# Kernel tuning notes

Measured on AMD Instinct MI355X. Metric: run time of the kernel, lower is better.

## Reference

```python
import jax, jax.numpy as jnp
import numpy as np

D_MODEL = 1024
NUM_HEADS = 16
D_K = D_MODEL // NUM_HEADS


def setup_inputs() -> dict:
    key = jax.random.key(0)
    ks = jax.random.split(key, 9)
    s = 1.0 / np.sqrt(D_MODEL)
    x = jax.random.normal(ks[0], (2, 2048, D_MODEL), dtype=jnp.float32)
    Wq = jax.random.uniform(ks[1], (D_MODEL, D_MODEL), jnp.float32, -s, s)
    bq = jax.random.uniform(ks[2], (D_MODEL,), jnp.float32, -s, s)
    Wk = jax.random.uniform(ks[3], (D_MODEL, D_MODEL), jnp.float32, -s, s)
    bk = jax.random.uniform(ks[4], (D_MODEL,), jnp.float32, -s, s)
    Wv = jax.random.uniform(ks[5], (D_MODEL, D_MODEL), jnp.float32, -s, s)
    bv = jax.random.uniform(ks[6], (D_MODEL,), jnp.float32, -s, s)
    Wo = jax.random.uniform(ks[7], (D_MODEL, D_MODEL), jnp.float32, -s, s)
    bo = jax.random.uniform(ks[8], (D_MODEL,), jnp.float32, -s, s)
    return {"x": x, "Wq": Wq, "bq": bq, "Wk": Wk, "bk": bk,
            "Wv": Wv, "bv": bv, "Wo": Wo, "bo": bo}


def reference(x, Wq, bq, Wk, bk, Wv, bv, Wo, bo):
    B, S, _ = x.shape
    # torch Linear: y = x @ W.T + b
    def proj(W, b):
        h = x @ W.T + b                       # [B,S,D]
        return h.reshape(B, S, NUM_HEADS, D_K).transpose(0, 2, 1, 3)  # [B,H,S,Dk]
    Q = proj(Wq, bq)
    K = proj(Wk, bk)
    V = proj(Wv, bv)
    scale = 1.0 / np.sqrt(D_K)
    scores = jnp.einsum('bhqd,bhkd->bhqk', Q, K) * scale   # [B,H,S,S]
    causal = jnp.triu(jnp.ones((S, S), dtype=bool), k=1)   # True above diag
    scores = jnp.where(causal, -jnp.inf, scores)
    probs = jax.nn.softmax(scores, axis=-1)
    out = jnp.einsum('bhqk,bhkd->bhqd', probs, V)          # [B,H,S,Dk]
    out = out.transpose(0, 2, 1, 3).reshape(B, S, NUM_HEADS * D_K)
    return out @ Wo.T + bo
```

## Files before the change

kernel.cpp:

```cpp
#include <hip/hip_runtime.h>

typedef unsigned short u16;
typedef __attribute__((ext_vector_type(8))) short short8;
typedef __attribute__((ext_vector_type(4))) float floatx4;

__device__ __forceinline__ u16 f2bf(float x){
  union { float f; unsigned u; } v; v.f = x;
  unsigned r = v.u + 0x7fffu + ((v.u >> 16) & 1u);
  return (u16)(r >> 16);
}

__device__ __forceinline__ unsigned cvt_pk_bf16(float lo, float hi){
  unsigned r;
  asm("v_cvt_pk_bf16_f32 %0, %1, %2" : "=v"(r) : "v"(lo), "v"(hi));
  return r;
}

__device__ __forceinline__ float exp2_raw(float x){
  float r;
  asm("v_exp_f32 %0, %1" : "=v"(r) : "v"(x));
  return r;
}

__device__ __forceinline__ void gld16(const u16* g, u16* l){
  __builtin_amdgcn_global_load_lds(
      (const __attribute__((address_space(1))) void*)g,
      (__attribute__((address_space(3))) void*)l, 16, 0, 0);
}

#define WAIT_BAR_V4() asm volatile("s_waitcnt vmcnt(4) lgkmcnt(0)\ns_barrier" ::: "memory")
#define WAIT_BAR_V3() asm volatile("s_waitcnt vmcnt(3) lgkmcnt(0)\ns_barrier" ::: "memory")
#define WAIT_BAR_V0() asm volatile("s_waitcnt vmcnt(0) lgkmcnt(0)\ns_barrier" ::: "memory")

__global__ void k_cvt_all(const float* __restrict__ x,
                          const float* __restrict__ wq, const float* __restrict__ wk,
                          const float* __restrict__ wv, const float* __restrict__ wo,
                          u16* __restrict__ xb, u16* __restrict__ wqb, u16* __restrict__ wkb,
                          u16* __restrict__ wvb, u16* __restrict__ wob){
  const int i = blockIdx.x * 256 + threadIdx.x;
  const float* s; u16* d; int off;
  if (i < 1048576) { s = x; d = xb; off = i; }
  else {
    const int j = i - 1048576;
    const int wsel = j >> 18;
    off = j & 262143;
    s = (wsel==0) ? wq : (wsel==1) ? wk : (wsel==2) ? wv : wo;
    d = (wsel==0) ? wqb : (wsel==1) ? wkb : (wsel==2) ? wvb : wob;
  }
  const float4 f = ((const float4*)s)[off];
  unsigned lo = (unsigned)f2bf(f.x) | ((unsigned)f2bf(f.y) << 16);
  unsigned hi = (unsigned)f2bf(f.z) | ((unsigned)f2bf(f.w) << 16);
  ((uint2*)d)[off] = make_uint2(lo, hi);
}

__global__ __launch_bounds__(256) void k_gemm_qkv(
    const u16* __restrict__ A,
    const u16* __restrict__ Wq, const u16* __restrict__ Wk, const u16* __restrict__ Wv,
    const float* __restrict__ bq, const float* __restrict__ bk, const float* __restrict__ bv,
    u16* __restrict__ Qo, u16* __restrict__ Ko, u16* __restrict__ Vo)
{
  const int bid = (int)blockIdx.x;
  const int xcd = bid & 7;
  const int i5  = bid >> 3;
  const int xb_ = ((xcd >> 2) << 2) + (i5 & 3);
  const int rest = i5 >> 2;
  const int yb_ = ((xcd & 3) << 3) + (rest & 7);
  const int mode = rest >> 3;

  const u16* W      = (mode==1) ? Wk : (mode==2) ? Wv : Wq;
  const float* bias = (mode==1) ? bk : (mode==2) ? bv : bq;

  __shared__ u16 lA[3][4096];
  __shared__ u16 lB[3][4096];

  const int tid  = threadIdx.x;
  const int row0 = yb_ * 128;
  const int col0 = xb_ * 128;

  const int srow = tid >> 2;
  const int sgp  = tid & 3;
  const int sgl  = sgp ^ ((srow >> 1) & 3);
  const u16* ga0 = A + (row0 + srow)      * 1024 + sgl * 8;
  const u16* ga1 = A + (row0 + srow + 64) * 1024 + sgl * 8;
  const u16* gb0 = W + (col0 + srow)      * 1024 + sgl * 8;
  const u16* gb1 = W + (col0 + srow + 64) * 1024 + sgl * 8;

  const int l  = tid & 63, w = tid >> 6;
  const int wr = w >> 1,  wc = w & 1;
  const int lr = l & 15,  grp = l >> 4;
  const int sw = (lr >> 1) & 3;
  int aoff[4], boff[4];
#pragma unroll
  for (int m = 0; m < 4; ++m) aoff[m] = (wr*64 + m*16 + lr)*32 + ((grp ^ sw) * 8);
#pragma unroll
  for (int n = 0; n < 4; ++n) boff[n] = (wc*64 + n*16 + lr)*32 + ((grp ^ sw) * 8);

  floatx4 acc[4][4];
#pragma unroll
  for (int m = 0; m < 4; ++m)
#pragma unroll
    for (int n = 0; n < 4; ++n) acc[m][n] = (floatx4){0.f, 0.f, 0.f, 0.f};

#define STAGE(buf, kt_) do { \
    const int k0_ = (kt_) * 32; \
    gld16(ga0 + k0_, &lA[(buf)][tid*8]); \
    gld16(ga1 + k0_, &lA[(buf)][2048 + tid*8]); \
    gld16(gb0 + k0_, &lB[(buf)][tid*8]); \
    gld16(gb1 + k0_, &lB[(buf)][2048 + tid*8]); \
  } while (0)

  STAGE(0, 0);
  STAGE(1, 1);
  asm volatile("s_waitcnt vmcnt(4)\ns_barrier" ::: "memory");

  for (int kt0 = 0; kt0 < 32; kt0 += 3) {
#pragma unroll
    for (int i = 0; i < 3; ++i) {
      const int kt = kt0 + i;
      if (kt >= 32) break;
      const bool st2 = (kt + 2 < 32);
      if (st2) STAGE((i + 2) % 3, kt + 2);
      short8 af[4], bf[4];
#pragma unroll
      for (int m = 0; m < 4; ++m) af[m] = *(const short8*)&lA[i][aoff[m]];
#pragma unroll
      for (int n = 0; n < 4; ++n) bf[n] = *(const short8*)&lB[i][boff[n]];
#pragma unroll
      for (int m = 0; m < 4; ++m)
#pragma unroll
        for (int n = 0; n < 4; ++n)
          acc[m][n] = __builtin_amdgcn_mfma_f32_16x16x32_bf16(af[m], bf[n], acc[m][n], 0, 0, 0);
      if (st2) WAIT_BAR_V4(); else WAIT_BAR_V0();
    }
  }
#undef STAGE

  const float sc = (mode == 0) ? 0.18033688011112042f : 1.0f;
  u16* dst = (mode == 0) ? Qo : (mode == 1) ? Ko : Vo;
#pragma unroll
  for (int n = 0; n < 4; ++n) {
    const int cg = col0 + wc*64 + n*16 + lr;
    const float bb = bias[cg];
    const int h = cg >> 6, d = cg & 63;
#pragma unroll
    for (int m = 0; m < 4; ++m) {
#pragma unroll
      for (int j = 0; j < 4; ++j) {
        const int rg = row0 + wr*64 + m*16 + grp*4 + j;
        const int b = rg >> 11, s5 = rg & 2047;
        const float val = (acc[m][n][j] + bb) * sc;
        int idx;
        if (mode == 2) idx = ((b*16 + h)*64 + d)*2048 + s5;
        else           idx = ((b*16 + h)*2048 + s5)*64 + d;
        dst[idx] = f2bf(val);
      }
    }
  }
}

__global__ __launch_bounds__(256) void k_gemm_o(
    const u16* __restrict__ A, const u16* __restrict__ W,
    const float* __restrict__ bias, float* __restrict__ Fo)
{
  const int bid = (int)blockIdx.x;
  const int xcd = bid & 7;
  const int i5  = bid >> 3;
  const int xb_ = ((xcd >> 2) << 2) + (i5 & 3);
  const int yb_ = ((xcd & 3) << 4) + (i5 >> 2);

  __shared__ u16 lA[3][2048];
  __shared__ u16 lB[3][4096];

  const int tid  = threadIdx.x;
  const int row0 = yb_ * 64;
  const int col0 = xb_ * 128;

  const int srow = tid >> 2;
  const int sgp  = tid & 3;
  const int sgl  = sgp ^ ((srow >> 1) & 3);
  const u16* ga0 = A + (row0 + srow)      * 1024 + sgl * 8;
  const u16* gb0 = W + (col0 + srow)      * 1024 + sgl * 8;
  const u16* gb1 = W + (col0 + srow + 64) * 1024 + sgl * 8;

  const int l  = tid & 63, w = tid >> 6;
  const int wr = w >> 1,  wc = w & 1;
  const int lr = l & 15,  grp = l >> 4;
  const int sw = (lr >> 1) & 3;
  int aoff[2], boff[4];
#pragma unroll
  for (int m = 0; m < 2; ++m) aoff[m] = (wr*32 + m*16 + lr)*32 + ((grp ^ sw) * 8);
#pragma unroll
  for (int n = 0; n < 4; ++n) boff[n] = (wc*64 + n*16 + lr)*32 + ((grp ^ sw) * 8);

  floatx4 acc[2][4];
#pragma unroll
  for (int m = 0; m < 2; ++m)
#pragma unroll
    for (int n = 0; n < 4; ++n) acc[m][n] = (floatx4){0.f, 0.f, 0.f, 0.f};

#define STAGE(buf, kt_) do { \
    const int k0_ = (kt_) * 32; \
    gld16(ga0 + k0_, &lA[(buf)][tid*8]); \
    gld16(gb0 + k0_, &lB[(buf)][tid*8]); \
    gld16(gb1 + k0_, &lB[(buf)][2048 + tid*8]); \
  } while (0)

  STAGE(0, 0);
  STAGE(1, 1);
  asm volatile("s_waitcnt vmcnt(3)\ns_barrier" ::: "memory");

  for (int kt0 = 0; kt0 < 32; kt0 += 3) {
#pragma unroll
    for (int i = 0; i < 3; ++i) {
      const int kt = kt0 + i;
      if (kt >= 32) break;
      const bool st2 = (kt + 2 < 32);
      if (st2) STAGE((i + 2) % 3, kt + 2);
      short8 af[2], bf[4];
#pragma unroll
      for (int m = 0; m < 2; ++m) af[m] = *(const short8*)&lA[i][aoff[m]];
#pragma unroll
      for (int n = 0; n < 4; ++n) bf[n] = *(const short8*)&lB[i][boff[n]];
#pragma unroll
      for (int m = 0; m < 2; ++m)
#pragma unroll
        for (int n = 0; n < 4; ++n)
          acc[m][n] = __builtin_amdgcn_mfma_f32_16x16x32_bf16(af[m], bf[n], acc[m][n], 0, 0, 0);
      if (st2) WAIT_BAR_V3(); else WAIT_BAR_V0();
    }
  }
#undef STAGE

#pragma unroll
  for (int n = 0; n < 4; ++n) {
    const int cg = col0 + wc*64 + n*16 + lr;
    const float bb = bias[cg];
#pragma unroll
    for (int m = 0; m < 2; ++m) {
      const int rg = row0 + wr*32 + m*16 + grp*4;
#pragma unroll
      for (int j = 0; j < 4; ++j)
        Fo[(rg + j) * 1024 + cg] = acc[m][n][j] + bb;
    }
  }
}

__global__ __launch_bounds__(256, 2) void k_attn(
    const u16* __restrict__ Q, const u16* __restrict__ K,
    const u16* __restrict__ V, u16* __restrict__ O)
{
  __shared__ u16 lK[3][4096];
  __shared__ u16 lV[3][4096];
  __shared__ u16 lP[4][1024];

  const int tid = threadIdx.x;
  const int bid = (int)blockIdx.x;
  const int xcd = bid & 7, r = bid >> 3;
  const int bh = xcd * 4 + (r >> 4);
  const int pr = r & 15;

  const int l = tid & 63, w = tid >> 6;
  const int lr = l & 15, grp = l >> 4;

  const u16* Qh = Q + (size_t)bh * 2048 * 64;
  const u16* Kh = K + (size_t)bh * 2048 * 64;
  const u16* Vh = V + (size_t)bh * 64 * 2048;

  const int srow = tid >> 3, sgp = tid & 7;
  const int sgl = sgp ^ (srow & 7);
  u16* lPw = &lP[w][0];
  const int swz = lr & 7;
  const int b = bh >> 4, h = bh & 15;

#define STAGEKV(buf, kt_) do { \
    gld16(Kh + ((kt_)*64 + srow     )*64 + sgl*8, &lK[(buf)][tid*8]); \
    gld16(Kh + ((kt_)*64 + srow + 32)*64 + sgl*8, &lK[(buf)][2048 + tid*8]); \
    gld16(Vh + (srow     )*2048 + (kt_)*64 + sgl*8, &lV[(buf)][tid*8]); \
    gld16(Vh + (srow + 32)*2048 + (kt_)*64 + sgl*8, &lV[(buf)][2048 + tid*8]); \
  } while (0)

#pragma unroll
  for (int pass = 0; pass < 2; ++pass) {
    const int qt = pass ? pr : (31 - pr);
    const int qw0 = qt * 64 + w * 16;
    const int nkt = qt + 1;

    short8 qf[2];
#pragma unroll
    for (int kk = 0; kk < 2; ++kk)
      qf[kk] = *(const short8*)(Qh + (qw0 + lr)*64 + kk*32 + grp*8);

    floatx4 accO[4];
    float mrow = -1e30f, lrow = 0.f;
#pragma unroll
    for (int dn = 0; dn < 4; ++dn) accO[dn] = (floatx4){0.f, 0.f, 0.f, 0.f};

    STAGEKV(0, 0);
    if (nkt > 1) {
      STAGEKV(1, 1);
      asm volatile("s_waitcnt vmcnt(4)\ns_barrier" ::: "memory");
    } else {
      asm volatile("s_waitcnt vmcnt(0)\ns_barrier" ::: "memory");
    }

    for (int kt0 = 0; kt0 < nkt; kt0 += 3) {
#pragma unroll
      for (int i = 0; i < 3; ++i) {
        const int kt = kt0 + i;
        if (kt >= nkt) break;
        const bool st2 = (kt + 2 < nkt);
        if (st2) STAGEKV((i + 2) % 3, kt + 2);
        const int kb = kt * 64;

        floatx4 st[4];
#pragma unroll
        for (int n = 0; n < 4; ++n) st[n] = (floatx4){0.f, 0.f, 0.f, 0.f};
#pragma unroll
        for (int n = 0; n < 4; ++n) {
          const int key = n*16 + lr;
#pragma unroll
          for (int kk = 0; kk < 2; ++kk) {
            const int gp = (kk*4 + grp) ^ (key & 7);
            short8 kf = *(const short8*)&lK[i][key*64 + gp*8];
            st[n] = __builtin_amdgcn_mfma_f32_16x16x32_bf16(kf, qf[kk], st[n], 0, 0, 0);
          }
        }

        const int lim = qw0 + lr - kb;
        if (63 > lim) {
#pragma unroll
          for (int n = 0; n < 4; ++n)
#pragma unroll
            for (int j = 0; j < 4; ++j)
              if (n*16 + grp*4 + j > lim) st[n][j] = -1e30f;
        }

        float mt = st[0][0];
#pragma unroll
        for (int n = 0; n < 4; ++n)
#pragma unroll
          for (int j = 0; j < 4; ++j) mt = fmaxf(mt, st[n][j]);
        if (!__all(mt <= mrow)) {
          float mg = fmaxf(mt, __shfl_xor(mt, 16));
          mg = fmaxf(mg, __shfl_xor(mg, 32));
          const float mn = fmaxf(mrow, mg);
          const float alpha = exp2_raw(mrow - mn);
          mrow = mn;
          lrow *= alpha;
#pragma unroll
          for (int dn = 0; dn < 4; ++dn) accO[dn] *= alpha;
        }
        float ps = 0.f;
#pragma unroll
        for (int n = 0; n < 4; ++n)
#pragma unroll
          for (int j = 0; j < 4; ++j) {
            const float p = exp2_raw(st[n][j] - mrow);
            st[n][j] = p;
            ps += p;
          }
        lrow += ps;

#pragma unroll
        for (int n = 0; n < 4; ++n)
#pragma unroll
          for (int p2 = 0; p2 < 2; ++p2) {
            const unsigned pk = cvt_pk_bf16(st[n][2*p2], st[n][2*p2+1]);
            const int pg = (2*n + (grp >> 1)) ^ swz;
            ((unsigned*)lPw)[lr*32 + pg*4 + (grp & 1)*2 + p2] = pk;
          }

        asm volatile("s_waitcnt lgkmcnt(0)" ::: "memory");

        short8 pa[2];
#pragma unroll
        for (int kk = 0; kk < 2; ++kk)
          pa[kk] = *(const short8*)&lPw[lr*64 + (((kk*4 + grp) ^ swz) * 8)];

#pragma unroll
        for (int dn = 0; dn < 4; ++dn) {
          const int d = dn*16 + lr;
#pragma unroll
          for (int kk = 0; kk < 2; ++kk) {
            const int gp = (kk*4 + grp) ^ (d & 7);
            short8 vf = *(const short8*)&lV[i][d*64 + gp*8];
            accO[dn] = __builtin_amdgcn_mfma_f32_16x16x32_bf16(vf, pa[kk], accO[dn], 0, 0, 0);
          }
        }

        if (st2) WAIT_BAR_V4(); else WAIT_BAR_V0();
      }
    }

    float lt = lrow + __shfl_xor(lrow, 16);
    lt += __shfl_xor(lt, 32);
    const float inv = 1.0f / lt;
    const int token = b*2048 + qw0 + lr;
#pragma unroll
    for (int dn = 0; dn < 4; ++dn)
#pragma unroll
      for (int p2 = 0; p2 < 2; ++p2) {
        const unsigned pk = cvt_pk_bf16(accO[dn][2*p2] * inv, accO[dn][2*p2+1] * inv);
        *(unsigned*)&O[token*1024 + h*64 + dn*16 + grp*4 + 2*p2] = pk;
      }
  }
#undef STAGEKV
}

extern "C" void kernel_launch(void* const* d_in, const int* in_sizes, int n_in,
                              void* d_out, int out_size, void* d_ws, size_t ws_size,
                              hipStream_t stream) {
  const float* x  = (const float*)d_in[0];
  const float* Wq = (const float*)d_in[1];
  const float* bq = (const float*)d_in[2];
  const float* Wk = (const float*)d_in[3];
  const float* bk = (const float*)d_in[4];
  const float* Wv = (const float*)d_in[5];
  const float* bv = (const float*)d_in[6];
  const float* Wo = (const float*)d_in[7];
  const float* bo = (const float*)d_in[8];
  float* out = (float*)d_out;

  char* ws = (char*)d_ws;
  u16* xb  = (u16*)(ws + 0);
  u16* wqb = (u16*)(ws + 8388608);
  u16* wkb = (u16*)(ws + 10485760);
  u16* wvb = (u16*)(ws + 12582912);
  u16* wob = (u16*)(ws + 14680064);
  u16* Qb  = (u16*)(ws + 16777216);
  u16* Kb  = (u16*)(ws + 25165824);
  u16* Vb  = (u16*)(ws + 33554432);
  u16* Ab  = (u16*)(ws + 41943040);

  k_cvt_all<<<dim3(8192), 256, 0, stream>>>(x, Wq, Wk, Wv, Wo, xb, wqb, wkb, wvb, wob);

  k_gemm_qkv<<<dim3(768), 256, 0, stream>>>(xb, wqb, wkb, wvb, bq, bk, bv, Qb, Kb, Vb);

  k_attn<<<dim3(512), 256, 0, stream>>>(Qb, Kb, Vb, Ab);

  k_gemm_o<<<dim3(512), 256, 0, stream>>>(Ab, wob, bo, out);
}
```

Before: 112.9 us.

## Split attention into one q-tile per block with double-buffered KV and higher occupancy

Result: faster. 110.4 us (-2.3%).

```diff
diff --git a/kernel.cpp b/kernel.cpp
--- a/kernel.cpp
+++ b/kernel.cpp
@@ -245,22 +245,25 @@
   }
 }
 
-__global__ __launch_bounds__(256, 2) void k_attn(
+__global__ __launch_bounds__(256, 4) void k_attn(
     const u16* __restrict__ Q, const u16* __restrict__ K,
     const u16* __restrict__ V, u16* __restrict__ O)
 {
-  __shared__ u16 lK[3][4096];
-  __shared__ u16 lV[3][4096];
+  __shared__ u16 lK[2][4096];
+  __shared__ u16 lV[2][4096];
   __shared__ u16 lP[4][1024];
 
   const int tid = threadIdx.x;
   const int bid = (int)blockIdx.x;
   const int xcd = bid & 7, r = bid >> 3;
-  const int bh = xcd * 4 + (r >> 4);
-  const int pr = r & 15;
+  const int k_ = r & 31, j_ = r >> 5;
+  const int bh = xcd * 4 + j_;
+  const int qt = (j_ & 1) ? k_ : (31 - k_);
 
   const int l = tid & 63, w = tid >> 6;
   const int lr = l & 15, grp = l >> 4;
+  const int qw0 = qt * 64 + w * 16;
+  const int nkt = qt + 1;
 
   const u16* Qh = Q + (size_t)bh * 2048 * 64;
   const u16* Kh = K + (size_t)bh * 2048 * 64;
@@ -279,131 +282,117 @@
     gld16(Vh + (srow + 32)*2048 + (kt_)*64 + sgl*8, &lV[(buf)][2048 + tid*8]); \
   } while (0)
 
-#pragma unroll
-  for (int pass = 0; pass < 2; ++pass) {
-    const int qt = pass ? pr : (31 - pr);
-    const int qw0 = qt * 64 + w * 16;
-    const int nkt = qt + 1;
-
-    short8 qf[2];
-#pragma unroll
-    for (int kk = 0; kk < 2; ++kk)
-      qf[kk] = *(const short8*)(Qh + (qw0 + lr)*64 + kk*32 + grp*8);
-
-    floatx4 accO[4];
-    float mrow = -1e30f, lrow = 0.f;
-#pragma unroll
-    for (int dn = 0; dn < 4; ++dn) accO[dn] = (floatx4){0.f, 0.f, 0.f, 0.f};
-
-    STAGEKV(0, 0);
-    if (nkt > 1) {
-      STAGEKV(1, 1);
-      asm volatile("s_waitcnt vmcnt(4)\ns_barrier" ::: "memory");
-    } else {
-      asm volatile("s_waitcnt vmcnt(0)\ns_barrier" ::: "memory");
-    }
-
-    for (int kt0 = 0; kt0 < nkt; kt0 += 3) {
-#pragma unroll
-      for (int i = 0; i < 3; ++i) {
-        const int kt = kt0 + i;
-        if (kt >= nkt) break;
-        const bool st2 = (kt + 2 < nkt);
-        if (st2) STAGEKV((i + 2) % 3, kt + 2);
-        const int kb = kt * 64;
-
-        floatx4 st[4];
-#pragma unroll
-        for (int n = 0; n < 4; ++n) st[n] = (floatx4){0.f, 0.f, 0.f, 0.f};
-#pragma unroll
-        for (int n = 0; n < 4; ++n) {
-          const int key = n*16 + lr;
-#pragma unroll
-          for (int kk = 0; kk < 2; ++kk) {
-            const int gp = (kk*4 + grp) ^ (key & 7);
-            short8 kf = *(const short8*)&lK[i][key*64 + gp*8];
-            st[n] = __builtin_amdgcn_mfma_f32_16x16x32_bf16(kf, qf[kk], st[n], 0, 0, 0);
-          }
+  short8 qf[2];
+#pragma unroll
+  for (int kk = 0; kk < 2; ++kk)
+    qf[kk] = *(const short8*)(Qh + (qw0 + lr)*64 + kk*32 + grp*8);
+
+  floatx4 accO[4];
+  float mrow = -1e30f, lrow = 0.f;
+#pragma unroll
+  for (int dn = 0; dn < 4; ++dn) accO[dn] = (floatx4){0.f, 0.f, 0.f, 0.f};
+
+  STAGEKV(0, 0);
+  __syncthreads();
+
+  for (int kt0 = 0; kt0 < nkt; kt0 += 2) {
+#pragma unroll
+    for (int i = 0; i < 2; ++i) {
+      const int kt = kt0 + i;
+      if (kt >= nkt) break;
+      if (kt + 1 < nkt) STAGEKV(i ^ 1, kt + 1);
+      const int kb = kt * 64;
+
+      floatx4 st[4];
+#pragma unroll
+      for (int n = 0; n < 4; ++n) st[n] = (floatx4){0.f, 0.f, 0.f, 0.f};
+#pragma unroll
+      for (int n = 0; n < 4; ++n) {
+        const int key = n*16 + lr;
+#pragma unroll
+        for (int kk = 0; kk < 2; ++kk) {
+          const int gp = (kk*4 + grp) ^ (key & 7);
+          short8 kf = *(const short8*)&lK[i][key*64 + gp*8];
+          st[n] = __builtin_amdgcn_mfma_f32_16x16x32_bf16(kf, qf[kk], st[n], 0, 0, 0);
         }
-
-        const int lim = qw0 + lr - kb;
-        if (63 > lim) {
-#pragma unroll
-          for (int n = 0; n < 4; ++n)
-#pragma unroll
-            for (int j = 0; j < 4; ++j)
-              if (n*16 + grp*4 + j > lim) st[n][j] = -1e30f;
+      }
+
+      const int lim = qw0 + lr - kb;
+      if (63 > lim) {
+#pragma unroll
+        for (int n = 0; n < 4; ++n)
+#pragma unroll
+          for (int jj = 0; jj < 4; ++jj)
+            if (n*16 + grp*4 + jj > lim) st[n][jj] = -1e30f;
+      }
+
+      float mt = st[0][0];
+#pragma unroll
+      for (int n = 0; n < 4; ++n)
+#pragma unroll
+        for (int jj = 0; jj < 4; ++jj) mt = fmaxf(mt, st[n][jj]);
+      if (!__all(mt <= mrow)) {
+        float mg = fmaxf(mt, __shfl_xor(mt, 16));
+        mg = fmaxf(mg, __shfl_xor(mg, 32));
+        const float mn = fmaxf(mrow, mg);
+        const float alpha = exp2_raw(mrow - mn);
+        mrow = mn;
+        lrow *= alpha;
+#pragma unroll
+        for (int dn = 0; dn < 4; ++dn) accO[dn] *= alpha;
+      }
+      float ps = 0.f;
+#pragma unroll
+      for (int n = 0; n < 4; ++n)
+#pragma unroll
+        for (int jj = 0; jj < 4; ++jj) {
+          const float p = exp2_raw(st[n][jj] - mrow);
+          st[n][jj] = p;
+          ps += p;
         }
-
-        float mt = st[0][0];
-#pragma unroll
-        for (int n = 0; n < 4; ++n)
-#pragma unroll
-          for (int j = 0; j < 4; ++j) mt = fmaxf(mt, st[n][j]);
-        if (!__all(mt <= mrow)) {
-          float mg = fmaxf(mt, __shfl_xor(mt, 16));
-          mg = fmaxf(mg, __shfl_xor(mg, 32));
-          const float mn = fmaxf(mrow, mg);
-          const float alpha = exp2_raw(mrow - mn);
-          mrow = mn;
-          lrow *= alpha;
-#pragma unroll
-          for (int dn = 0; dn < 4; ++dn) accO[dn] *= alpha;
+      lrow += ps;
+
+#pragma unroll
+      for (int n = 0; n < 4; ++n)
+#pragma unroll
+        for (int p2 = 0; p2 < 2; ++p2) {
+          const unsigned pk = cvt_pk_bf16(st[n][2*p2], st[n][2*p2+1]);
+          const int pg = (2*n + (grp >> 1)) ^ swz;
+          ((unsigned*)lPw)[lr*32 + pg*4 + (grp & 1)*2 + p2] = pk;
         }
-        float ps = 0.f;
-#pragma unroll
-        for (int n = 0; n < 4; ++n)
-#pragma unroll
-          for (int j = 0; j < 4; ++j) {
-            const float p = exp2_raw(st[n][j] - mrow);
-            st[n][j] = p;
-            ps += p;
-          }
-        lrow += ps;
-
-#pragma unroll
-        for (int n = 0; n < 4; ++n)
-#pragma unroll
-          for (int p2 = 0; p2 < 2; ++p2) {
-            const unsigned pk = cvt_pk_bf16(st[n][2*p2], st[n][2*p2+1]);
-            const int pg = (2*n + (grp >> 1)) ^ swz;
-            ((unsigned*)lPw)[lr*32 + pg*4 + (grp & 1)*2 + p2] = pk;
-          }
-
-        asm volatile("s_waitcnt lgkmcnt(0)" ::: "memory");
-
-        short8 pa[2];
-#pragma unroll
-        for (int kk = 0; kk < 2; ++kk)
-          pa[kk] = *(const short8*)&lPw[lr*64 + (((kk*4 + grp) ^ swz) * 8)];
-
-#pragma unroll
-        for (int dn = 0; dn < 4; ++dn) {
-          const int d = dn*16 + lr;
-#pragma unroll
-          for (int kk = 0; kk < 2; ++kk) {
-            const int gp = (kk*4 + grp) ^ (d & 7);
-            short8 vf = *(const short8*)&lV[i][d*64 + gp*8];
-            accO[dn] = __builtin_amdgcn_mfma_f32_16x16x32_bf16(vf, pa[kk], accO[dn], 0, 0, 0);
-          }
+
+      asm volatile("s_waitcnt lgkmcnt(0)" ::: "memory");
+
+      short8 pa[2];
+#pragma unroll
+      for (int kk = 0; kk < 2; ++kk)
+        pa[kk] = *(const short8*)&lPw[lr*64 + (((kk*4 + grp) ^ swz) * 8)];
+
+#pragma unroll
+      for (int dn = 0; dn < 4; ++dn) {
+        const int d = dn*16 + lr;
+#pragma unroll
+        for (int kk = 0; kk < 2; ++kk) {
+          const int gp = (kk*4 + grp) ^ (d & 7);
+          short8 vf = *(const short8*)&lV[i][d*64 + gp*8];
+          accO[dn] = __builtin_amdgcn_mfma_f32_16x16x32_bf16(vf, pa[kk], accO[dn], 0, 0, 0);
         }
-
-        if (st2) WAIT_BAR_V4(); else WAIT_BAR_V0();
       }
-    }
-
-    float lt = lrow + __shfl_xor(lrow, 16);
-    lt += __shfl_xor(lt, 32);
-    const float inv = 1.0f / lt;
-    const int token = b*2048 + qw0 + lr;
-#pragma unroll
-    for (int dn = 0; dn < 4; ++dn)
-#pragma unroll
-      for (int p2 = 0; p2 < 2; ++p2) {
-        const unsigned pk = cvt_pk_bf16(accO[dn][2*p2] * inv, accO[dn][2*p2+1] * inv);
-        *(unsigned*)&O[token*1024 + h*64 + dn*16 + grp*4 + 2*p2] = pk;
-      }
-  }
+      __syncthreads();
+    }
+  }
+
+  float lt = lrow + __shfl_xor(lrow, 16);
+  lt += __shfl_xor(lt, 32);
+  const float inv = 1.0f / lt;
+  const int token = b*2048 + qw0 + lr;
+#pragma unroll
+  for (int dn = 0; dn < 4; ++dn)
+#pragma unroll
+    for (int p2 = 0; p2 < 2; ++p2) {
+      const unsigned pk = cvt_pk_bf16(accO[dn][2*p2] * inv, accO[dn][2*p2+1] * inv);
+      *(unsigned*)&O[token*1024 + h*64 + dn*16 + grp*4 + 2*p2] = pk;
+    }
 #undef STAGEKV
 }
 
@@ -436,7 +425,7 @@
 
   k_gemm_qkv<<<dim3(768), 256, 0, stream>>>(xb, wqb, wkb, wvb, bq, bk, bv, Qb, Kb, Vb);
 
-  k_attn<<<dim3(512), 256, 0, stream>>>(Qb, Kb, Vb, Ab);
+  k_attn<<<dim3(1024), 256, 0, stream>>>(Qb, Kb, Vb, Ab);
 
   k_gemm_o<<<dim3(512), 256, 0, stream>>>(Ab, wob, bo, out);
 }
```
